# Kernel optimization log

Measured on AMD Instinct MI355X. Metric: run time of the kernel, lower is better.

## Reference

```python
import jax, jax.numpy as jnp
import numpy as np

TEMPERATURE = 0.5
BATCH_SIZE = 4096
EPS = 1e-8  # torch.nn.CosineSimilarity default eps


def setup_inputs() -> dict:
    key = jax.random.key(0)
    k1, k2 = jax.random.split(key)
    z1 = jax.random.normal(k1, (BATCH_SIZE, 256), dtype=jnp.float32)
    z2 = jax.random.normal(k2, (BATCH_SIZE, 256), dtype=jnp.float32)
    return {"z1": z1, "z2": z2}


def reference(z1, z2):
    B = z1.shape[0]
    N = 2 * B
    reps = jnp.concatenate([z1, z2], axis=0)  # [N, D]
    # Cosine similarity (torch clamps each norm to eps before dividing)
    norms = jnp.maximum(jnp.linalg.norm(reps, axis=1, keepdims=True), EPS)
    z = reps / norms
    sim = z @ z.T  # [N, N] cosine similarity matrix

    # positives: diagonals at offsets +B and -B (they are identical by symmetry,
    # but keep the original concat order: [diag(+B), diag(-B)])
    l_pos = jnp.diagonal(sim, offset=B)
    r_pos = jnp.diagonal(sim, offset=-B)
    positives = jnp.concatenate([l_pos, r_pos])  # [N]

    inv_t = 1.0 / TEMPERATURE
    pos_logit = positives * inv_t  # logits[:, 0]

    # negatives are all off-diagonal entries of each row (the positive pair is
    # thus present twice in the logits, faithful to the original). CE with
    # label 0 => loss_i = logsumexp(logits_i) - logits_i[0].
    neg_logits = jnp.where(jnp.eye(N, dtype=bool), -jnp.inf, sim * inv_t)
    lse = jnp.logaddexp(pos_logit, jax.scipy.special.logsumexp(neg_logits, axis=1))
    loss = jnp.sum(lse - pos_logit) / N
    return loss
```

## Files before the change

kernel.cpp:

```cpp
#include <hip/hip_runtime.h>
#include <hip/hip_bf16.h>
#include <cstdint>
#include <cstddef>
#include <math.h>

#define BSZ   4096
#define NROW  8192
#define DIM   256
#define INV_T 2.0f
#define EPS_N 1e-8f

typedef __attribute__((ext_vector_type(8))) short bf16x8;
typedef __attribute__((ext_vector_type(4))) float f32x4;

__device__ __forceinline__ unsigned short f2bf(float x) {
    __hip_bfloat16 h = __float2bfloat16(x);
    return __builtin_bit_cast(unsigned short, h);
}

__device__ __forceinline__ void load_lds16(const void* g, void* l) {
    __builtin_amdgcn_global_load_lds(
        (const __attribute__((address_space(1))) void*)g,
        (__attribute__((address_space(3))) void*)l,
        16, 0, 0);
}

__global__ __launch_bounds__(256)
void nt_normalize(const float* __restrict__ z1,
                  const float* __restrict__ z2,
                  char* __restrict__ zn2,
                  float* __restrict__ rowsum) {
    const int wave = threadIdx.x >> 6;
    const int lane = threadIdx.x & 63;
    const int row  = blockIdx.x * 4 + wave;
    const float* src = (row < BSZ) ? (z1 + (size_t)row * DIM)
                                   : (z2 + (size_t)(row - BSZ) * DIM);
    const float4 v = ((const float4*)src)[lane];
    float ss = v.x * v.x + v.y * v.y + v.z * v.z + v.w * v.w;
    #pragma unroll
    for (int off = 32; off; off >>= 1) ss += __shfl_xor(ss, off);
    const float rinv = 1.0f / fmaxf(sqrtf(ss), EPS_N);
    ushort4 o;
    o.x = f2bf(v.x * rinv);
    o.y = f2bf(v.y * rinv);
    o.z = f2bf(v.z * rinv);
    o.w = f2bf(v.w * rinv);
    const int s    = row >> 7;
    const int lrow = row & 127;
    const int kc   = lane >> 4;
    const int unit = (lane >> 1) & 7;
    const int half = lane & 1;
    const int u    = unit ^ (lrow & 7);
    *(ushort4*)(zn2 + (size_t)s * 65536 + kc * 16384 + lrow * 128 + u * 16 + half * 8) = o;
    if (lane == 0) rowsum[row] = 0.0f;
}

__global__ __launch_bounds__(256)
void nt_gram(const char* __restrict__ zn2,
             float* __restrict__ rowsum,
             float* __restrict__ pos) {
    const int l = blockIdx.x;
    int bi = (int)((129.0 - sqrt(16641.0 - 8.0 * (double)l)) * 0.5);
    while (64 * (bi + 1) - (bi + 1) * bi / 2 <= l) ++bi;
    while (64 * bi - bi * (bi - 1) / 2 > l) --bi;
    const int bj = bi + (l - (64 * bi - bi * (bi - 1) / 2));

    __shared__ char Bs[16384];

    const int t    = threadIdx.x;
    const int lane = t & 63;
    const int wave = t >> 6;
    const int wrow = (wave >> 1) * 64;
    const int wcol = (wave & 1) * 64;
    const int q    = lane >> 4;
    const int r16  = lane & 15;
    const int sw   = r16 & 7;
    const int t16  = t * 16;

    const char* A2 = zn2 + (size_t)bi * 65536;
    const char* B2 = zn2 + (size_t)bj * 65536;

    f32x4 acc[4][4] = {};

    for (int kc = 0; kc < 4; ++kc) {
        #pragma unroll
        for (int p = 0; p < 4; ++p)
            load_lds16(B2 + kc * 16384 + p * 4096 + t16, Bs + p * 4096 + t16);

        bf16x8 af[2][4];
        #pragma unroll
        for (int kh = 0; kh < 2; ++kh) {
            const int cpos = (((kh << 2) + q) ^ sw) << 4;
            #pragma unroll
            for (int mi = 0; mi < 4; ++mi)
                af[kh][mi] = *(const bf16x8*)(
                    A2 + kc * 16384 + (wrow + mi * 16 + r16) * 128 + cpos);
        }
        __syncthreads();

        #pragma unroll
        for (int kh = 0; kh < 2; ++kh) {
            const int cpos = (((kh << 2) + q) ^ sw) << 4;
            bf16x8 bfv[4];
            #pragma unroll
            for (int ni = 0; ni < 4; ++ni)
                bfv[ni] = *(const bf16x8*)(Bs + (wcol + ni * 16 + r16) * 128 + cpos);
            #pragma unroll
            for (int mi = 0; mi < 4; ++mi)
                #pragma unroll
                for (int ni = 0; ni < 4; ++ni)
                    acc[mi][ni] = __builtin_amdgcn_mfma_f32_16x16x32_bf16(
                        af[kh][mi], bfv[ni], acc[mi][ni], 0, 0, 0);
        }
        __syncthreads();
    }

    const int c = r16;
    const bool diag_block = (bi == bj);
    float colp[4] = {0.f, 0.f, 0.f, 0.f};

    #pragma unroll
    for (int mi = 0; mi < 4; ++mi) {
        #pragma unroll
        for (int r = 0; r < 4; ++r) {
            const int grow = bi * 128 + wrow + mi * 16 + q * 4 + r;
            float s = 0.f;
            #pragma unroll
            for (int ni = 0; ni < 4; ++ni) {
                const int gcol = bj * 128 + wcol + ni * 16 + c;
                const float val = acc[mi][ni][r];
                float e = __expf(val * INV_T);
                e = (grow == gcol) ? 0.f : e;
                s += e;
                colp[ni] += e;
                if (gcol == grow + BSZ) {
                    pos[grow] = val;
                    pos[gcol] = val;
                }
            }
            s += __shfl_xor(s, 1);
            s += __shfl_xor(s, 2);
            s += __shfl_xor(s, 4);
            s += __shfl_xor(s, 8);
            if (c == 0) atomicAdd(&rowsum[grow], s);
        }
    }
    if (!diag_block) {
        #pragma unroll
        for (int ni = 0; ni < 4; ++ni) {
            float cs = colp[ni];
            cs += __shfl_xor(cs, 16);
            cs += __shfl_xor(cs, 32);
            if (q == 0) atomicAdd(&rowsum[bj * 128 + wcol + ni * 16 + c], cs);
        }
    }
}

__global__ __launch_bounds__(1024)
void nt_finalize(const float* __restrict__ rowsum,
                 const float* __restrict__ pos,
                 float* __restrict__ out) {
    const float4* rs4 = (const float4*)rowsum;
    const float4* ps4 = (const float4*)pos;
    float v = 0.f;
    #pragma unroll
    for (int it = 0; it < 2; ++it) {
        const int i = it * 1024 + threadIdx.x;
        const float4 r = rs4[i];
        const float4 p = ps4[i];
        v += logf(__expf(p.x * INV_T) + r.x) - p.x * INV_T;
        v += logf(__expf(p.y * INV_T) + r.y) - p.y * INV_T;
        v += logf(__expf(p.z * INV_T) + r.z) - p.z * INV_T;
        v += logf(__expf(p.w * INV_T) + r.w) - p.w * INV_T;
    }
    #pragma unroll
    for (int off = 32; off; off >>= 1) v += __shfl_xor(v, off);
    __shared__ float redf[16];
    if ((threadIdx.x & 63) == 0) redf[threadIdx.x >> 6] = v;
    __syncthreads();
    if (threadIdx.x == 0) {
        float s = 0.f;
        #pragma unroll
        for (int w = 0; w < 16; ++w) s += redf[w];
        out[0] = s * (1.0f / NROW);
    }
}

extern "C" void kernel_launch(void* const* d_in, const int* in_sizes, int n_in,
                              void* d_out, int out_size, void* d_ws, size_t ws_size,
                              hipStream_t stream) {
    const float* z1 = (const float*)d_in[0];
    const float* z2 = (const float*)d_in[1];
    float* out = (float*)d_out;

    char*  zn2    = (char*)d_ws;
    float* rowsum = (float*)((char*)d_ws + (size_t)NROW * DIM * 2);
    float* pos    = rowsum + NROW;

    nt_normalize<<<NROW / 4, 256, 0, stream>>>(z1, z2, zn2, rowsum);
    nt_gram<<<2080, 256, 0, stream>>>(zn2, rowsum, pos);
    nt_finalize<<<1, 1024, 0, stream>>>(rowsum, pos, out);
}
```

Baseline: 109.5 us.

## Switch Gram matrix to FP8 MFMA with halved-size swizzled operand layout

Normalized embeddings are now quantized to FP8 instead of BF16, halving the stored operand size and workspace footprint. The Gram kernel uses the fp8 16x16x32 MFMA and stages both A and B tiles through LDS with async global-to-LDS loads, rather than reading A straight from global into registers. The aim is to cut memory traffic and raise matrix throughput. The cost is lower precision in the cosine similarities, which are then exponentiated, so the loss may drift from the reference.

```diff
diff --git a/kernel.cpp b/kernel.cpp
--- a/kernel.cpp
+++ b/kernel.cpp
@@ -10,13 +10,7 @@
 #define INV_T 2.0f
 #define EPS_N 1e-8f
 
-typedef __attribute__((ext_vector_type(8))) short bf16x8;
 typedef __attribute__((ext_vector_type(4))) float f32x4;
-
-__device__ __forceinline__ unsigned short f2bf(float x) {
-    __hip_bfloat16 h = __float2bfloat16(x);
-    return __builtin_bit_cast(unsigned short, h);
-}
 
 __device__ __forceinline__ void load_lds16(const void* g, void* l) {
     __builtin_amdgcn_global_load_lds(
@@ -28,7 +22,7 @@
 __global__ __launch_bounds__(256)
 void nt_normalize(const float* __restrict__ z1,
                   const float* __restrict__ z2,
-                  char* __restrict__ zn2,
+                  char* __restrict__ zn3,
                   float* __restrict__ rowsum) {
     const int wave = threadIdx.x >> 6;
     const int lane = threadIdx.x & 63;
@@ -40,23 +34,21 @@
     #pragma unroll
     for (int off = 32; off; off >>= 1) ss += __shfl_xor(ss, off);
     const float rinv = 1.0f / fmaxf(sqrtf(ss), EPS_N);
-    ushort4 o;
-    o.x = f2bf(v.x * rinv);
-    o.y = f2bf(v.y * rinv);
-    o.z = f2bf(v.z * rinv);
-    o.w = f2bf(v.w * rinv);
+    int pk = 0;
+    pk = __builtin_amdgcn_cvt_pk_fp8_f32(v.x * rinv, v.y * rinv, pk, false);
+    pk = __builtin_amdgcn_cvt_pk_fp8_f32(v.z * rinv, v.w * rinv, pk, true);
     const int s    = row >> 7;
     const int lrow = row & 127;
     const int kc   = lane >> 4;
     const int unit = (lane >> 1) & 7;
-    const int half = lane & 1;
+    const int off4 = (lane & 1) * 4;
     const int u    = unit ^ (lrow & 7);
-    *(ushort4*)(zn2 + (size_t)s * 65536 + kc * 16384 + lrow * 128 + u * 16 + half * 8) = o;
+    *(int*)(zn3 + (size_t)s * 32768 + kc * 8192 + lrow * 64 + u * 8 + off4) = pk;
     if (lane == 0) rowsum[row] = 0.0f;
 }
 
 __global__ __launch_bounds__(256)
-void nt_gram(const char* __restrict__ zn2,
+void nt_gram(const char* __restrict__ zn3,
              float* __restrict__ rowsum,
              float* __restrict__ pos) {
     const int l = blockIdx.x;
@@ -65,7 +57,8 @@
     while (64 * bi - bi * (bi - 1) / 2 > l) --bi;
     const int bj = bi + (l - (64 * bi - bi * (bi - 1) / 2));
 
-    __shared__ char Bs[16384];
+    __shared__ char As[8192];
+    __shared__ char Bs[8192];
 
     const int t    = threadIdx.x;
     const int lane = t & 63;
@@ -77,40 +70,34 @@
     const int sw   = r16 & 7;
     const int t16  = t * 16;
 
-    const char* A2 = zn2 + (size_t)bi * 65536;
-    const char* B2 = zn2 + (size_t)bj * 65536;
+    const char* A2 = zn3 + (size_t)bi * 32768;
+    const char* B2 = zn3 + (size_t)bj * 32768;
 
     f32x4 acc[4][4] = {};
 
     for (int kc = 0; kc < 4; ++kc) {
-        #pragma unroll
-        for (int p = 0; p < 4; ++p)
-            load_lds16(B2 + kc * 16384 + p * 4096 + t16, Bs + p * 4096 + t16);
-
-        bf16x8 af[2][4];
-        #pragma unroll
-        for (int kh = 0; kh < 2; ++kh) {
-            const int cpos = (((kh << 2) + q) ^ sw) << 4;
-            #pragma unroll
-            for (int mi = 0; mi < 4; ++mi)
-                af[kh][mi] = *(const bf16x8*)(
-                    A2 + kc * 16384 + (wrow + mi * 16 + r16) * 128 + cpos);
-        }
+        load_lds16(A2 + kc * 8192 + t16,        As + t16);
+        load_lds16(A2 + kc * 8192 + 4096 + t16, As + 4096 + t16);
+        load_lds16(B2 + kc * 8192 + t16,        Bs + t16);
+        load_lds16(B2 + kc * 8192 + 4096 + t16, Bs + 4096 + t16);
         __syncthreads();
 
         #pragma unroll
         for (int kh = 0; kh < 2; ++kh) {
-            const int cpos = (((kh << 2) + q) ^ sw) << 4;
-            bf16x8 bfv[4];
+            const int spos = (((kh << 2) + q) ^ sw) << 3;
+            long af[4], bfv[4];
+            #pragma unroll
+            for (int mi = 0; mi < 4; ++mi)
+                af[mi] = *(const long*)(As + (wrow + mi * 16 + r16) * 64 + spos);
             #pragma unroll
             for (int ni = 0; ni < 4; ++ni)
-                bfv[ni] = *(const bf16x8*)(Bs + (wcol + ni * 16 + r16) * 128 + cpos);
+                bfv[ni] = *(const long*)(Bs + (wcol + ni * 16 + r16) * 64 + spos);
             #pragma unroll
             for (int mi = 0; mi < 4; ++mi)
                 #pragma unroll
                 for (int ni = 0; ni < 4; ++ni)
-                    acc[mi][ni] = __builtin_amdgcn_mfma_f32_16x16x32_bf16(
-                        af[kh][mi], bfv[ni], acc[mi][ni], 0, 0, 0);
+                    acc[mi][ni] = __builtin_amdgcn_mfma_f32_16x16x32_fp8_fp8(
+                        af[mi], bfv[ni], acc[mi][ni], 0, 0, 0);
         }
         __syncthreads();
     }
@@ -193,11 +180,11 @@
     const float* z2 = (const float*)d_in[1];
     float* out = (float*)d_out;
 
-    char*  zn2    = (char*)d_ws;
-    float* rowsum = (float*)((char*)d_ws + (size_t)NROW * DIM * 2);
+    char*  zn3    = (char*)d_ws;
+    float* rowsum = (float*)((char*)d_ws + (size_t)NROW * DIM);
     float* pos    = rowsum + NROW;
 
-    nt_normalize<<<NROW / 4, 256, 0, stream>>>(z1, z2, zn2, rowsum);
-    nt_gram<<<2080, 256, 0, stream>>>(zn2, rowsum, pos);
+    nt_normalize<<<NROW / 4, 256, 0, stream>>>(z1, z2, zn3, rowsum);
+    nt_gram<<<2080, 256, 0, stream>>>(zn3, rowsum, pos);
     nt_finalize<<<1, 1024, 0, stream>>>(rowsum, pos, out);
 }
```

New measurement: 100.8 us. 7.9% less time.
